# Kernel tuning notes

Hardware: AMD Instinct MI355X
Metric: run time of the kernel (lower is better)

The kernel has to match this reference:

```python
import jax, jax.numpy as jnp
import numpy as np

N_NODES = 70000
N_EDGES = 2_000_000
IN_CH, FEAT_CH, OUT_CH = 1044, 128, 3


def _gcn_norm(src_sl, dst_sl, n_nodes, dtype):
    # PyG gcn_norm with add_self_loops=True, edge_weight=1:
    # deg over target nodes, norm = deg^-1/2[src] * deg^-1/2[dst]
    deg = jax.ops.segment_sum(jnp.ones(src_sl.shape[0], dtype=dtype), dst_sl,
                              num_segments=n_nodes)
    dinv = jnp.where(deg > 0, jax.lax.rsqrt(deg), jnp.zeros((), dtype))
    return dinv[src_sl] * dinv[dst_sl]


def _gcn_layer(x, src_sl, dst_sl, norm, W, b, n_nodes):
    h = x @ W                                  # [N, out] linear transform first
    msg = h[src_sl] * norm[:, None]            # gather + scale
    out = jax.ops.segment_sum(msg, dst_sl, num_segments=n_nodes)  # scatter-add
    return out + b


def setup_inputs() -> dict:
    key = jax.random.key(0)
    ks = jax.random.split(key, 6)
    features = jax.random.normal(ks[0], (N_NODES, IN_CH), dtype=jnp.float32)
    edges = jax.random.randint(ks[1], (2, N_EDGES), 0, N_NODES, dtype=jnp.int64)
    edges2 = jax.random.randint(ks[2], (2, N_EDGES), 0, N_NODES, dtype=jnp.int64)
    edge_features = jax.random.normal(ks[3], (N_EDGES,), dtype=jnp.float32)
    W1 = jax.random.normal(ks[4], (IN_CH, FEAT_CH), dtype=jnp.float32) * (1.0 / np.sqrt(IN_CH))
    b1 = jnp.zeros((FEAT_CH,), dtype=jnp.float32)
    W2 = jax.random.normal(ks[5], (FEAT_CH, OUT_CH), dtype=jnp.float32) * (1.0 / np.sqrt(FEAT_CH))
    b2 = jnp.zeros((OUT_CH,), dtype=jnp.float32)
    return {"features": features, "edges": edges, "edges2": edges2,
            "edge_features": edge_features, "W1": W1, "b1": b1, "W2": W2, "b2": b2}


def reference(features, edges, edges2, edge_features, W1, b1, W2, b2):
    # edge_features is discarded by the module (set to None); edges2 unused.
    n = features.shape[0]
    loop = jnp.arange(n, dtype=edges.dtype)
    src_sl = jnp.concatenate([edges[0], loop])  # self-loops appended
    dst_sl = jnp.concatenate([edges[1], loop])
    norm = _gcn_norm(src_sl, dst_sl, n, features.dtype)
    x = _gcn_layer(features, src_sl, dst_sl, norm, W1, b1, n)
    x = jax.nn.relu(x)
    # dropout is identity in eval mode (deterministic reference)
    return _gcn_layer(x, src_sl, dst_sl, norm, W2, b2, n)
```

## Files before the change

### kernel.cpp

```cpp
#include <hip/hip_runtime.h>
#include <hip/hip_bf16.h>

#define K_IN   1044
#define N_FEAT 128
#define KPAD2  1088
#define NST2   17
#define BM     96

#define NB     512
#define BWMAX  256
#define EPB    8192

typedef __attribute__((ext_vector_type(8))) short short8;
typedef __attribute__((ext_vector_type(4))) float f32x4;

__device__ __forceinline__ ushort f2bf(float f) {
  unsigned x = __float_as_uint(f);
  x += 0x7fffu + ((x >> 16) & 1u);
  return (ushort)(x >> 16);
}
__device__ __forceinline__ uint pkbf(float lo, float hi) {
  __hip_bfloat162 h = __float22bfloat162_rn(make_float2(lo, hi));
  return *reinterpret_cast<uint*>(&h);
}
__device__ __forceinline__ float bflo(uint v) { return __uint_as_float(v << 16); }
__device__ __forceinline__ float bfhi(uint v) { return __uint_as_float(v & 0xFFFF0000u); }

__device__ __forceinline__ uint divbw(uint d, uint M32) { return __umulhi(d, M32); }

__device__ __forceinline__ void gld16(const void* g, void* l) {
  __builtin_amdgcn_global_load_lds(
      (const __attribute__((address_space(1))) unsigned int*)g,
      (__attribute__((address_space(3))) unsigned int*)l, 16, 0, 0);
}


__global__ __launch_bounds__(256) void convw1_hist_kernel(const float* __restrict__ W1,
                                                          ushort* __restrict__ W1T,
                                                          const int* __restrict__ dst,
                                                          int* __restrict__ pbc,
                                                          int E, int bw, uint M32,
                                                          int convBlocks, int eblocks) {
  if ((int)blockIdx.x < convBlocks) {
    int idx = blockIdx.x * 256 + threadIdx.x;
    if (idx >= N_FEAT * KPAD2) return;
    int col = idx / KPAD2, k = idx - col * KPAD2;
    int kk = k & ~63;
    int jp = (k >> 3) & 7;
    int e  = k & 7;
    int jl = jp ^ (col & 7);
    int ksrc = kk + 8 * jl + e;
    W1T[idx] = (ksrc < K_IN) ? f2bf(W1[(size_t)ksrc * N_FEAT + col]) : (ushort)0;
  } else {
    __shared__ int h[NB];
    const int t = threadIdx.x;
    const int blk = blockIdx.x - convBlocks;
    for (int i = t; i < NB; i += 256) h[i] = 0;
    __syncthreads();
    const int e0 = blk * EPB;
    const int e1 = min(e0 + EPB, E);
    for (int e = e0 + t; e < e1; e += 256) atomicAdd(&h[divbw((uint)dst[e], M32)], 1);
    __syncthreads();
    for (int i = t; i < NB; i += 256) pbc[i * eblocks + blk] = h[i];
  }
}

__global__ __launch_bounds__(256) void csr_scan_bucket_kernel(int* __restrict__ pbc,
                                                              int* __restrict__ bt,
                                                              int eblocks) {
  __shared__ int sc[256];
  const int b = blockIdx.x;
  const int t = threadIdx.x;
  int v = (t < eblocks) ? pbc[(size_t)b * eblocks + t] : 0;
  sc[t] = v;
  __syncthreads();
  for (int off = 1; off < 256; off <<= 1) {
    int x = (t >= off) ? sc[t - off] : 0;
    __syncthreads();
    sc[t] += x;
    __syncthreads();
  }
  if (t < eblocks) pbc[(size_t)b * eblocks + t] = sc[t] - v;
  if (t == 255) bt[b] = sc[255];
}

__global__ __launch_bounds__(256) void csr_stage_kernel(const int* __restrict__ src,
                                                        const int* __restrict__ dst,
                                                        const int* __restrict__ pbc,
                                                        const int* __restrict__ bt,
                                                        uint* __restrict__ staging, int E, int bw,
                                                        uint M32, int eblocks) {
  __shared__ int sc[256];
  __shared__ int cur[NB];
  const int t = threadIdx.x;
  const int blk = blockIdx.x;
  int v0 = bt[2 * t], v1 = bt[2 * t + 1];
  int s = v0 + v1;
  sc[t] = s;
  __syncthreads();
  for (int off = 1; off < 256; off <<= 1) {
    int x = (t >= off) ? sc[t - off] : 0;
    __syncthreads();
    sc[t] += x;
    __syncthreads();
  }
  int excl = sc[t] - s;
  cur[2 * t]     = excl      + pbc[(size_t)(2 * t) * eblocks + blk];
  cur[2 * t + 1] = excl + v0 + pbc[(size_t)(2 * t + 1) * eblocks + blk];
  __syncthreads();
  const int e0 = blk * EPB;
  const int e1 = min(e0 + EPB, E);
  for (int e = e0 + t; e < e1; e += 256) {
    int d = dst[e];
    int b = (int)divbw((uint)d, M32);
    int p = atomicAdd(&cur[b], 1);
    staging[p] = ((uint)src[e] << 8) | (uint)(d - b * bw);
  }
}

__global__ __launch_bounds__(256) void csr_final_kernel(const uint* __restrict__ staging,
                                                        const int* __restrict__ bt,
                                                        int* __restrict__ row_ptr,
                                                        int* __restrict__ sorted_src,
                                                        float* __restrict__ dinv,
                                                        int N, int bw, int E) {
  __shared__ int hist[BWMAX];
  __shared__ int sc[256];
  __shared__ int bb[NB];
  const int b = blockIdx.x;
  const int t = threadIdx.x;
  if (b == 0 && t == 0) row_ptr[N] = E;

  {
    int v0 = bt[2 * t], v1 = bt[2 * t + 1];
    int s = v0 + v1;
    sc[t] = s;
    __syncthreads();
    for (int off = 1; off < 256; off <<= 1) {
      int x = (t >= off) ? sc[t - off] : 0;
      __syncthreads();
      sc[t] += x;
      __syncthreads();
    }
    int excl = sc[t] - s;
    bb[2 * t]     = excl;
    bb[2 * t + 1] = excl + v0;
    __syncthreads();
  }

  const int node0 = b * bw;
  const int nn = min(bw, N - node0);
  if (nn <= 0) return;
  const int base = bb[b];
  const int cnt  = bt[b];

  for (int i = t; i < BWMAX; i += 256) hist[i] = 0;
  __syncthreads();
  for (int i = t; i < cnt; i += 256)
    atomicAdd(&hist[staging[base + i] & 255u], 1);
  __syncthreads();
  int v = (t < nn) ? hist[t] : 0;
  if (t < nn) dinv[node0 + t] = rsqrtf((float)(v + 1));
  sc[t] = v;
  __syncthreads();
  for (int off = 1; off < 256; off <<= 1) {
    int x = (t >= off) ? sc[t - off] : 0;
    __syncthreads();
    sc[t] += x;
    __syncthreads();
  }
  int excl = sc[t] - v;
  if (t < nn) row_ptr[node0 + t] = base + excl;
  if (t < nn) hist[t] = excl;
  __syncthreads();
  for (int i = t; i < cnt; i += 256) {
    uint p = staging[base + i];
    int c = atomicAdd(&hist[p & 255u], 1);
    sorted_src[base + c] = (int)(p >> 8);
  }
}


__global__ __launch_bounds__(256) void gemm1_mfma_kernel(const float* __restrict__ X,
                                                         const ushort* __restrict__ W1T,
                                                         const float* __restrict__ dinv,
                                                         ushort* __restrict__ G1, int M) {
  __shared__ float  Af[2][BM * 64];
  __shared__ ushort Bsb[2][128 * 64];

  const int t = threadIdx.x;
  const int row0 = blockIdx.x * BM;
  const int w = t >> 6, l = t & 63;
  const int w24 = w * 24, w32 = w * 32;
  const int Mm1 = M - 1;

  const int wm = w >> 1, wn = w & 1;
  const int lr = l & 15, g = l >> 4;

  f32x4 acc[3][4] = {};

  auto stage = [&](int s, int buf) {
    const int kk = s * 64;
    #pragma unroll
    for (int i = 0; i < 6; i++) {
      int r  = w24 + 4 * i + (l >> 4);
      int jl = (l & 15) ^ (r & 15);
      int grow = min(row0 + r, Mm1);
      int gk   = min(kk + 4 * jl, K_IN - 4);
      gld16(X + (size_t)grow * K_IN + gk, (void*)&Af[buf][(w24 + 4 * i) * 64]);
    }
    #pragma unroll
    for (int i = 0; i < 4; i++) {
      int c = w32 + 8 * i + (l >> 3);
      gld16(W1T + (size_t)c * KPAD2 + kk + 8 * (l & 7),
            (void*)&Bsb[buf][(w32 + 8 * i) * 64]);
    }
  };

  stage(0, 0);
  __syncthreads();

  int cur = 0;
  #pragma unroll 1
  for (int s = 0; s < NST2; s++) {
    if (s + 1 < NST2) stage(s + 1, cur ^ 1);

    #pragma unroll
    for (int ss = 0; ss < 2; ss++) {
      short8 af[3], bfr[4];
      #pragma unroll
      for (int m = 0; m < 3; m++) {
        const int row = wm * 48 + m * 16 + lr;
        const float* rp = &Af[cur][row * 64];
        const int c0 = (ss * 8 + 2 * g)     ^ (row & 15);
        const int c1 = (ss * 8 + 2 * g + 1) ^ (row & 15);
        float4 a0 = *(const float4*)&rp[c0 * 4];
        float4 a1 = *(const float4*)&rp[c1 * 4];
        uint4 uu = make_uint4(pkbf(a0.x, a0.y), pkbf(a0.z, a0.w),
                              pkbf(a1.x, a1.y), pkbf(a1.z, a1.w));
        af[m] = *(short8*)&uu;
      }
      #pragma unroll
      for (int n = 0; n < 4; n++) {
        const int col = wn * 64 + n * 16 + lr;
        const int cB = (ss * 4 + g) ^ (col & 7);
        bfr[n] = *(const short8*)&Bsb[cur][col * 64 + cB * 8];
      }
      #pragma unroll
      for (int m = 0; m < 3; m++)
        #pragma unroll
        for (int n = 0; n < 4; n++)
          acc[m][n] = __builtin_amdgcn_mfma_f32_16x16x32_bf16(af[m], bfr[n], acc[m][n], 0, 0, 0);
    }

    __syncthreads();
    cur ^= 1;
  }

  const int rbase = row0 + wm * 48 + g * 4;
  const int cbase = wn * 64 + lr;
  #pragma unroll
  for (int m = 0; m < 3; m++) {
    #pragma unroll
    for (int r = 0; r < 4; r++) {
      int row = rbase + m * 16 + r;
      if (row < M) {
        float dv = dinv[row];
        #pragma unroll
        for (int n = 0; n < 4; n++)
          G1[(size_t)row * N_FEAT + cbase + n * 16] = f2bf(dv * acc[m][n][r]);
      }
    }
  }
}


__global__ __launch_bounds__(256) void agg1mm_kernel(const ushort* __restrict__ G1,
                                                     const int* __restrict__ row_ptr,
                                                     const int* __restrict__ sorted_src,
                                                     const float* __restrict__ dinv,
                                                     const float* __restrict__ b1,
                                                     const float* __restrict__ W2,
                                                     float* __restrict__ G2, int N) {
  const int w = (blockIdx.x * blockDim.x + threadIdx.x) >> 6;
  const int lane = threadIdx.x & 63;
  if (w >= N) return;
  const int beg = row_ptr[w], end = row_ptr[w + 1];
  const uint* g1u = (const uint*)G1;
  const int co = lane;

  uint vs = g1u[((size_t)w << 6) + co];
  float a0 = bflo(vs), a1 = bfhi(vs);

  int e = beg;
  for (; e + 16 <= end; e += 16) {
    int s[16];
    #pragma unroll
    for (int i = 0; i < 16; i++) s[i] = sorted_src[e + i];
    uint v[16];
    #pragma unroll
    for (int i = 0; i < 16; i++) v[i] = g1u[((size_t)s[i] << 6) + co];
    #pragma unroll
    for (int i = 0; i < 16; i++) { a0 += bflo(v[i]); a1 += bfhi(v[i]); }
  }
  for (; e + 4 <= end; e += 4) {
    int s[4];
    #pragma unroll
    for (int i = 0; i < 4; i++) s[i] = sorted_src[e + i];
    uint v[4];
    #pragma unroll
    for (int i = 0; i < 4; i++) v[i] = g1u[((size_t)s[i] << 6) + co];
    #pragma unroll
    for (int i = 0; i < 4; i++) { a0 += bflo(v[i]); a1 += bfhi(v[i]); }
  }
  for (; e < end; e++) {
    uint v = g1u[((size_t)sorted_src[e] << 6) + co];
    a0 += bflo(v); a1 += bfhi(v);
  }

  const float di = dinv[w];
  float r0 = fmaxf(fmaf(di, a0, b1[2 * co + 0]), 0.f);
  float r1 = fmaxf(fmaf(di, a1, b1[2 * co + 1]), 0.f);

  const float* wrow = W2 + 6 * co;
  float s0 = r0 * wrow[0] + r1 * wrow[3];
  float s1 = r0 * wrow[1] + r1 * wrow[4];
  float s2 = r0 * wrow[2] + r1 * wrow[5];
  #pragma unroll
  for (int off = 32; off > 0; off >>= 1) {
    s0 += __shfl_down(s0, off);
    s1 += __shfl_down(s1, off);
    s2 += __shfl_down(s2, off);
  }
  if (lane == 0) {
    *(float4*)&G2[(size_t)w * 4] = make_float4(di * s0, di * s1, di * s2, 0.f);
  }
}


__global__ __launch_bounds__(256) void agg2_kernel(const float* __restrict__ G2,
                                                   const int* __restrict__ row_ptr,
                                                   const int* __restrict__ sorted_src,
                                                   const float* __restrict__ dinv,
                                                   const float* __restrict__ b2,
                                                   float* __restrict__ out, int N) {
  int t = blockIdx.x * blockDim.x + threadIdx.x;
  int node = t >> 4, lane = t & 15;
  if (node >= N) return;
  int beg = row_ptr[node], end = row_ptr[node + 1];
  float a0 = 0.f, a1 = 0.f, a2 = 0.f;
  for (int e = beg + lane; e < end; e += 16) {
    float4 v = *(const float4*)&G2[(size_t)sorted_src[e] * 4];
    a0 += v.x; a1 += v.y; a2 += v.z;
  }
  #pragma unroll
  for (int off = 8; off > 0; off >>= 1) {
    a0 += __shfl_down(a0, off, 16);
    a1 += __shfl_down(a1, off, 16);
    a2 += __shfl_down(a2, off, 16);
  }
  if (lane == 0) {
    float di = dinv[node];
    float4 self = *(const float4*)&G2[(size_t)node * 4];
    out[node * 3 + 0] = di * (a0 + self.x) + b2[0];
    out[node * 3 + 1] = di * (a1 + self.y) + b2[1];
    out[node * 3 + 2] = di * (a2 + self.z) + b2[2];
  }
}


extern "C" void kernel_launch(void* const* d_in, const int* in_sizes, int n_in,
                              void* d_out, int out_size, void* d_ws, size_t ws_size,
                              hipStream_t stream) {
  const float* features = (const float*)d_in[0];
  const int*   edges    = (const int*)d_in[1];
  const float* W1 = (const float*)d_in[4];
  const float* b1 = (const float*)d_in[5];
  const float* W2 = (const float*)d_in[6];
  const float* b2 = (const float*)d_in[7];
  float* out = (float*)d_out;

  const int N = in_sizes[0] / K_IN;
  const int E = in_sizes[1] / 2;
  const int* src = edges;
  const int* dst = edges + E;
  const int bw = (N + NB - 1) / NB;
  const uint M32 = (uint)((0x100000000ULL + (unsigned long long)bw - 1) / (unsigned long long)bw);

  char* ws = (char*)d_ws;
  size_t off = 0;
  auto alloc = [&](size_t bytes) {
    void* p = ws + off;
    off += (bytes + 255) & ~(size_t)255;
    return p;
  };
  const int eblocks = (E + EPB - 1) / EPB;

  int*    pbc           = (int*)   alloc((size_t)NB * eblocks * sizeof(int));
  int*    bt            = (int*)   alloc((size_t)NB * sizeof(int));
  int*    row_ptr       = (int*)   alloc((size_t)(N + 1) * sizeof(int));
  float*  dinv          = (float*) alloc((size_t)N * sizeof(float));
  uint*   staging       = (uint*)  alloc((size_t)E * sizeof(uint));
  int*    sorted_src    = (int*)   alloc((size_t)E * sizeof(int));
  ushort* G1            = (ushort*)alloc((size_t)N * N_FEAT * sizeof(ushort));
  float*  G2            = (float*) alloc((size_t)N * 4 * sizeof(float));
  ushort* W1T           = (ushort*)alloc((size_t)N_FEAT * KPAD2 * sizeof(ushort));
  (void)ws_size;

  const int convBlocks = (N_FEAT * KPAD2 + 255) / 256;

  convw1_hist_kernel<<<convBlocks + eblocks, 256, 0, stream>>>(W1, W1T, dst, pbc, E, bw, M32, convBlocks, eblocks);
  csr_scan_bucket_kernel<<<NB, 256, 0, stream>>>(pbc, bt, eblocks);
  csr_stage_kernel<<<eblocks, 256, 0, stream>>>(src, dst, pbc, bt, staging, E, bw, M32, eblocks);
  csr_final_kernel<<<NB, 256, 0, stream>>>(staging, bt, row_ptr, sorted_src, dinv, N, bw, E);
  gemm1_mfma_kernel<<<(N + BM - 1) / BM, 256, 0, stream>>>(features, W1T, dinv, G1, N);
  agg1mm_kernel<<<((size_t)N * 64 + 255) / 256, 256, 0, stream>>>(G1, row_ptr, sorted_src, dinv, b1, W2, G2, N);
  agg2_kernel<<<((size_t)N * 16 + 255) / 256, 256, 0, stream>>>(G2, row_ptr, sorted_src, dinv, b2, out, N);
}
```

Measured before the change: 234.0 us.

## Fuse four CSR-build kernels into one persistent kernel with grid barriers

Merges the W1 conversion/histogram, bucket scan, staging scatter and final per-bucket sort kernels into a single 512-block persistent kernel that separates phases with a software grid barrier built on global atomics. The aim is to remove three kernel launch gaps and their tail effects between small CSR phases. It adds a memset for the barrier counter, relies on all 512 blocks being co-resident to avoid deadlock, and adds barrier spin and fence costs.

```diff
diff --git a/kernel.cpp b/kernel.cpp
--- a/kernel.cpp
+++ b/kernel.cpp
@@ -7,9 +7,10 @@
 #define NST2   17
 #define BM     96
 
-#define NB     512
-#define BWMAX  256
-#define EPB    8192
+#define NB      512
+#define BWMAX   256
+#define EPB     8192
+#define CSRGRID 512
 
 typedef __attribute__((ext_vector_type(8))) short short8;
 typedef __attribute__((ext_vector_type(4))) float f32x4;
@@ -34,102 +35,110 @@
       (__attribute__((address_space(3))) unsigned int*)l, 16, 0, 0);
 }
 
-
-__global__ __launch_bounds__(256) void convw1_hist_kernel(const float* __restrict__ W1,
-                                                          ushort* __restrict__ W1T,
-                                                          const int* __restrict__ dst,
-                                                          int* __restrict__ pbc,
-                                                          int E, int bw, uint M32,
-                                                          int convBlocks, int eblocks) {
-  if ((int)blockIdx.x < convBlocks) {
-    int idx = blockIdx.x * 256 + threadIdx.x;
-    if (idx >= N_FEAT * KPAD2) return;
-    int col = idx / KPAD2, k = idx - col * KPAD2;
-    int kk = k & ~63;
-    int jp = (k >> 3) & 7;
-    int e  = k & 7;
-    int jl = jp ^ (col & 7);
-    int ksrc = kk + 8 * jl + e;
-    W1T[idx] = (ksrc < K_IN) ? f2bf(W1[(size_t)ksrc * N_FEAT + col]) : (ushort)0;
-  } else {
-    __shared__ int h[NB];
-    const int t = threadIdx.x;
-    const int blk = blockIdx.x - convBlocks;
-    for (int i = t; i < NB; i += 256) h[i] = 0;
+__device__ __forceinline__ void gridbar(int* __restrict__ bar) {
+  __syncthreads();
+  if (threadIdx.x == 0) {
+    __threadfence();
+    int g = __hip_atomic_load(&bar[1], __ATOMIC_RELAXED, __HIP_MEMORY_SCOPE_AGENT);
+    int a = __hip_atomic_fetch_add(&bar[0], 1, __ATOMIC_ACQ_REL, __HIP_MEMORY_SCOPE_AGENT);
+    if (a == CSRGRID - 1) {
+      __hip_atomic_store(&bar[0], 0, __ATOMIC_RELAXED, __HIP_MEMORY_SCOPE_AGENT);
+      __hip_atomic_fetch_add(&bar[1], 1, __ATOMIC_ACQ_REL, __HIP_MEMORY_SCOPE_AGENT);
+    } else {
+      while (__hip_atomic_load(&bar[1], __ATOMIC_ACQUIRE, __HIP_MEMORY_SCOPE_AGENT) == g)
+        __builtin_amdgcn_s_sleep(8);
+    }
+    __threadfence();
+  }
+  __syncthreads();
+}
+
+
+__global__ __launch_bounds__(256) void csr_mega_kernel(const float* __restrict__ W1,
+                                                       ushort* __restrict__ W1T,
+                                                       const int* __restrict__ src,
+                                                       const int* __restrict__ dst,
+                                                       int* __restrict__ pbc,
+                                                       int* __restrict__ bt,
+                                                       uint* __restrict__ staging,
+                                                       int* __restrict__ row_ptr,
+                                                       int* __restrict__ sorted_src,
+                                                       float* __restrict__ dinv,
+                                                       int N, int E, int bw, uint M32,
+                                                       int convBlocks, int eblocks,
+                                                       int* __restrict__ bar) {
+  __shared__ int h[NB];
+  __shared__ int sc[256];
+  __shared__ int hist2[BWMAX];
+  const int t = threadIdx.x;
+  const int blk = blockIdx.x;
+
+  for (int vb = blk; vb < convBlocks + eblocks; vb += CSRGRID) {
+    if (vb < convBlocks) {
+      int idx = vb * 256 + t;
+      if (idx < N_FEAT * KPAD2) {
+        int col = idx / KPAD2, k = idx - col * KPAD2;
+        int kk = k & ~63;
+        int jp = (k >> 3) & 7;
+        int e  = k & 7;
+        int jl = jp ^ (col & 7);
+        int ksrc = kk + 8 * jl + e;
+        W1T[idx] = (ksrc < K_IN) ? f2bf(W1[(size_t)ksrc * N_FEAT + col]) : (ushort)0;
+      }
+    } else {
+      const int c = vb - convBlocks;
+      for (int i = t; i < NB; i += 256) h[i] = 0;
+      __syncthreads();
+      const int e0 = c * EPB;
+      const int e1 = min(e0 + EPB, E);
+      for (int e = e0 + t; e < e1; e += 256) atomicAdd(&h[divbw((uint)dst[e], M32)], 1);
+      __syncthreads();
+      for (int i = t; i < NB; i += 256) pbc[(size_t)i * eblocks + c] = h[i];
+      __syncthreads();
+    }
+  }
+  gridbar(bar);
+
+  {
+    int v = (t < eblocks) ? pbc[(size_t)blk * eblocks + t] : 0;
+    sc[t] = v;
+    __syncthreads();
+    for (int off = 1; off < 256; off <<= 1) {
+      int x = (t >= off) ? sc[t - off] : 0;
+      __syncthreads();
+      sc[t] += x;
+      __syncthreads();
+    }
+    if (t < eblocks) pbc[(size_t)blk * eblocks + t] = sc[t] - v;
+    if (t == 255) bt[blk] = sc[255];
+  }
+  gridbar(bar);
+
+  if (blk < eblocks) {
+    int v0 = bt[2 * t], v1 = bt[2 * t + 1];
+    int s = v0 + v1;
+    sc[t] = s;
+    __syncthreads();
+    for (int off = 1; off < 256; off <<= 1) {
+      int x = (t >= off) ? sc[t - off] : 0;
+      __syncthreads();
+      sc[t] += x;
+      __syncthreads();
+    }
+    int excl = sc[t] - s;
+    h[2 * t]     = excl      + pbc[(size_t)(2 * t) * eblocks + blk];
+    h[2 * t + 1] = excl + v0 + pbc[(size_t)(2 * t + 1) * eblocks + blk];
     __syncthreads();
     const int e0 = blk * EPB;
     const int e1 = min(e0 + EPB, E);
-    for (int e = e0 + t; e < e1; e += 256) atomicAdd(&h[divbw((uint)dst[e], M32)], 1);
-    __syncthreads();
-    for (int i = t; i < NB; i += 256) pbc[i * eblocks + blk] = h[i];
-  }
-}
-
-__global__ __launch_bounds__(256) void csr_scan_bucket_kernel(int* __restrict__ pbc,
-                                                              int* __restrict__ bt,
-                                                              int eblocks) {
-  __shared__ int sc[256];
-  const int b = blockIdx.x;
-  const int t = threadIdx.x;
-  int v = (t < eblocks) ? pbc[(size_t)b * eblocks + t] : 0;
-  sc[t] = v;
-  __syncthreads();
-  for (int off = 1; off < 256; off <<= 1) {
-    int x = (t >= off) ? sc[t - off] : 0;
-    __syncthreads();
-    sc[t] += x;
-    __syncthreads();
-  }
-  if (t < eblocks) pbc[(size_t)b * eblocks + t] = sc[t] - v;
-  if (t == 255) bt[b] = sc[255];
-}
-
-__global__ __launch_bounds__(256) void csr_stage_kernel(const int* __restrict__ src,
-                                                        const int* __restrict__ dst,
-                                                        const int* __restrict__ pbc,
-                                                        const int* __restrict__ bt,
-                                                        uint* __restrict__ staging, int E, int bw,
-                                                        uint M32, int eblocks) {
-  __shared__ int sc[256];
-  __shared__ int cur[NB];
-  const int t = threadIdx.x;
-  const int blk = blockIdx.x;
-  int v0 = bt[2 * t], v1 = bt[2 * t + 1];
-  int s = v0 + v1;
-  sc[t] = s;
-  __syncthreads();
-  for (int off = 1; off < 256; off <<= 1) {
-    int x = (t >= off) ? sc[t - off] : 0;
-    __syncthreads();
-    sc[t] += x;
-    __syncthreads();
-  }
-  int excl = sc[t] - s;
-  cur[2 * t]     = excl      + pbc[(size_t)(2 * t) * eblocks + blk];
-  cur[2 * t + 1] = excl + v0 + pbc[(size_t)(2 * t + 1) * eblocks + blk];
-  __syncthreads();
-  const int e0 = blk * EPB;
-  const int e1 = min(e0 + EPB, E);
-  for (int e = e0 + t; e < e1; e += 256) {
-    int d = dst[e];
-    int b = (int)divbw((uint)d, M32);
-    int p = atomicAdd(&cur[b], 1);
-    staging[p] = ((uint)src[e] << 8) | (uint)(d - b * bw);
-  }
-}
-
-__global__ __launch_bounds__(256) void csr_final_kernel(const uint* __restrict__ staging,
-                                                        const int* __restrict__ bt,
-                                                        int* __restrict__ row_ptr,
-                                                        int* __restrict__ sorted_src,
-                                                        float* __restrict__ dinv,
-                                                        int N, int bw, int E) {
-  __shared__ int hist[BWMAX];
-  __shared__ int sc[256];
-  __shared__ int bb[NB];
-  const int b = blockIdx.x;
-  const int t = threadIdx.x;
-  if (b == 0 && t == 0) row_ptr[N] = E;
+    for (int e = e0 + t; e < e1; e += 256) {
+      int d = dst[e];
+      int b = (int)divbw((uint)d, M32);
+      int p = atomicAdd(&h[b], 1);
+      staging[p] = ((uint)src[e] << 8) | (uint)(d - b * bw);
+    }
+  }
+  gridbar(bar);
 
   {
     int v0 = bt[2 * t], v1 = bt[2 * t + 1];
@@ -143,23 +152,23 @@
       __syncthreads();
     }
     int excl = sc[t] - s;
-    bb[2 * t]     = excl;
-    bb[2 * t + 1] = excl + v0;
-    __syncthreads();
-  }
-
-  const int node0 = b * bw;
+    h[2 * t]     = excl;
+    h[2 * t + 1] = excl + v0;
+    __syncthreads();
+  }
+  if (blk == 0 && t == 0) row_ptr[N] = E;
+  const int node0 = blk * bw;
   const int nn = min(bw, N - node0);
   if (nn <= 0) return;
-  const int base = bb[b];
-  const int cnt  = bt[b];
-
-  for (int i = t; i < BWMAX; i += 256) hist[i] = 0;
+  const int base = h[blk];
+  const int cnt  = bt[blk];
+
+  for (int i = t; i < BWMAX; i += 256) hist2[i] = 0;
   __syncthreads();
   for (int i = t; i < cnt; i += 256)
-    atomicAdd(&hist[staging[base + i] & 255u], 1);
-  __syncthreads();
-  int v = (t < nn) ? hist[t] : 0;
+    atomicAdd(&hist2[staging[base + i] & 255u], 1);
+  __syncthreads();
+  int v = (t < nn) ? hist2[t] : 0;
   if (t < nn) dinv[node0 + t] = rsqrtf((float)(v + 1));
   sc[t] = v;
   __syncthreads();
@@ -171,11 +180,11 @@
   }
   int excl = sc[t] - v;
   if (t < nn) row_ptr[node0 + t] = base + excl;
-  if (t < nn) hist[t] = excl;
+  if (t < nn) hist2[t] = excl;
   __syncthreads();
   for (int i = t; i < cnt; i += 256) {
     uint p = staging[base + i];
-    int c = atomicAdd(&hist[p & 255u], 1);
+    int c = atomicAdd(&hist2[p & 255u], 1);
     sorted_src[base + c] = (int)(p >> 8);
   }
 }
@@ -396,6 +405,7 @@
   };
   const int eblocks = (E + EPB - 1) / EPB;
 
+  int*    bar           = (int*)   alloc(64);
   int*    pbc           = (int*)   alloc((size_t)NB * eblocks * sizeof(int));
   int*    bt            = (int*)   alloc((size_t)NB * sizeof(int));
   int*    row_ptr       = (int*)   alloc((size_t)(N + 1) * sizeof(int));
@@ -409,10 +419,10 @@
 
   const int convBlocks = (N_FEAT * KPAD2 + 255) / 256;
 
-  convw1_hist_kernel<<<convBlocks + eblocks, 256, 0, stream>>>(W1, W1T, dst, pbc, E, bw, M32, convBlocks, eblocks);
-  csr_scan_bucket_kernel<<<NB, 256, 0, stream>>>(pbc, bt, eblocks);
-  csr_stage_kernel<<<eblocks, 256, 0, stream>>>(src, dst, pbc, bt, staging, E, bw, M32, eblocks);
-  csr_final_kernel<<<NB, 256, 0, stream>>>(staging, bt, row_ptr, sorted_src, dinv, N, bw, E);
+  hipMemsetAsync(bar, 0, 64, stream);
+  csr_mega_kernel<<<CSRGRID, 256, 0, stream>>>(W1, W1T, src, dst, pbc, bt, staging,
+                                               row_ptr, sorted_src, dinv,
+                                               N, E, bw, M32, convBlocks, eblocks, bar);
   gemm1_mfma_kernel<<<(N + BM - 1) / BM, 256, 0, stream>>>(features, W1T, dinv, G1, N);
   agg1mm_kernel<<<((size_t)N * 64 + 255) / 256, 256, 0, stream>>>(G1, row_ptr, sorted_src, dinv, b1, W2, G2, N);
   agg2_kernel<<<((size_t)N * 16 + 255) / 256, 256, 0, stream>>>(G2, row_ptr, sorted_src, dinv, b2, out, N);
```

Measured after the change: 626.9 us. 2.68x slower.

## Merge CSR staging with GEMM1 launch and move source-degree scaling into aggregation

Applied to the files above, without the earlier changes.

The CSR staging pass and the first GEMM now run in one launch, with block ID ranges selecting the role, so the bandwidth-bound GEMM can overlap the atomic-heavy edge bucketing. To drop GEMM1's dependency on dinv, the per-source dinv scaling moves out of the GEMM epilogue into agg1mm, which now gathers dinv[src] per edge and uses FMA. This removes one launch and the serialization between CSR build and GEMM, but adds 2M extra scattered dinv loads in aggregation and a bf16 rounding change, since G1 is stored unscaled.

```diff
diff --git a/kernel.cpp b/kernel.cpp
--- a/kernel.cpp
+++ b/kernel.cpp
@@ -84,54 +84,26 @@
   if (t == 255) bt[b] = sc[255];
 }
 
-__global__ __launch_bounds__(256) void csr_stage_kernel(const int* __restrict__ src,
-                                                        const int* __restrict__ dst,
-                                                        const int* __restrict__ pbc,
-                                                        const int* __restrict__ bt,
-                                                        uint* __restrict__ staging, int E, int bw,
-                                                        uint M32, int eblocks) {
-  __shared__ int sc[256];
-  __shared__ int cur[NB];
+
+__global__ __launch_bounds__(256) void stage_gemm1_kernel(const int* __restrict__ src,
+                                                          const int* __restrict__ dst,
+                                                          const int* __restrict__ pbc,
+                                                          const int* __restrict__ bt,
+                                                          uint* __restrict__ staging,
+                                                          const float* __restrict__ X,
+                                                          const ushort* __restrict__ W1T,
+                                                          ushort* __restrict__ G1,
+                                                          int M, int E, int bw, uint M32,
+                                                          int eblocks) {
+  __shared__ float  Af[2][BM * 64];
+  __shared__ ushort Bsb[2][128 * 64];
+
   const int t = threadIdx.x;
-  const int blk = blockIdx.x;
-  int v0 = bt[2 * t], v1 = bt[2 * t + 1];
-  int s = v0 + v1;
-  sc[t] = s;
-  __syncthreads();
-  for (int off = 1; off < 256; off <<= 1) {
-    int x = (t >= off) ? sc[t - off] : 0;
-    __syncthreads();
-    sc[t] += x;
-    __syncthreads();
-  }
-  int excl = sc[t] - s;
-  cur[2 * t]     = excl      + pbc[(size_t)(2 * t) * eblocks + blk];
-  cur[2 * t + 1] = excl + v0 + pbc[(size_t)(2 * t + 1) * eblocks + blk];
-  __syncthreads();
-  const int e0 = blk * EPB;
-  const int e1 = min(e0 + EPB, E);
-  for (int e = e0 + t; e < e1; e += 256) {
-    int d = dst[e];
-    int b = (int)divbw((uint)d, M32);
-    int p = atomicAdd(&cur[b], 1);
-    staging[p] = ((uint)src[e] << 8) | (uint)(d - b * bw);
-  }
-}
-
-__global__ __launch_bounds__(256) void csr_final_kernel(const uint* __restrict__ staging,
-                                                        const int* __restrict__ bt,
-                                                        int* __restrict__ row_ptr,
-                                                        int* __restrict__ sorted_src,
-                                                        float* __restrict__ dinv,
-                                                        int N, int bw, int E) {
-  __shared__ int hist[BWMAX];
-  __shared__ int sc[256];
-  __shared__ int bb[NB];
-  const int b = blockIdx.x;
-  const int t = threadIdx.x;
-  if (b == 0 && t == 0) row_ptr[N] = E;
-
-  {
+
+  if ((int)blockIdx.x < eblocks) {
+    int* sc  = (int*)&Bsb[0][0];
+    int* cur = (int*)&Af[0][0];
+    const int blk = blockIdx.x;
     int v0 = bt[2 * t], v1 = bt[2 * t + 1];
     int s = v0 + v1;
     sc[t] = s;
@@ -143,53 +115,21 @@
       __syncthreads();
     }
     int excl = sc[t] - s;
-    bb[2 * t]     = excl;
-    bb[2 * t + 1] = excl + v0;
-    __syncthreads();
-  }
-
-  const int node0 = b * bw;
-  const int nn = min(bw, N - node0);
-  if (nn <= 0) return;
-  const int base = bb[b];
-  const int cnt  = bt[b];
-
-  for (int i = t; i < BWMAX; i += 256) hist[i] = 0;
-  __syncthreads();
-  for (int i = t; i < cnt; i += 256)
-    atomicAdd(&hist[staging[base + i] & 255u], 1);
-  __syncthreads();
-  int v = (t < nn) ? hist[t] : 0;
-  if (t < nn) dinv[node0 + t] = rsqrtf((float)(v + 1));
-  sc[t] = v;
-  __syncthreads();
-  for (int off = 1; off < 256; off <<= 1) {
-    int x = (t >= off) ? sc[t - off] : 0;
-    __syncthreads();
-    sc[t] += x;
-    __syncthreads();
-  }
-  int excl = sc[t] - v;
-  if (t < nn) row_ptr[node0 + t] = base + excl;
-  if (t < nn) hist[t] = excl;
-  __syncthreads();
-  for (int i = t; i < cnt; i += 256) {
-    uint p = staging[base + i];
-    int c = atomicAdd(&hist[p & 255u], 1);
-    sorted_src[base + c] = (int)(p >> 8);
-  }
-}
-
-
-__global__ __launch_bounds__(256) void gemm1_mfma_kernel(const float* __restrict__ X,
-                                                         const ushort* __restrict__ W1T,
-                                                         const float* __restrict__ dinv,
-                                                         ushort* __restrict__ G1, int M) {
-  __shared__ float  Af[2][BM * 64];
-  __shared__ ushort Bsb[2][128 * 64];
-
-  const int t = threadIdx.x;
-  const int row0 = blockIdx.x * BM;
+    cur[2 * t]     = excl      + pbc[(size_t)(2 * t) * eblocks + blk];
+    cur[2 * t + 1] = excl + v0 + pbc[(size_t)(2 * t + 1) * eblocks + blk];
+    __syncthreads();
+    const int e0 = blk * EPB;
+    const int e1 = min(e0 + EPB, E);
+    for (int e = e0 + t; e < e1; e += 256) {
+      int d = dst[e];
+      int b = (int)divbw((uint)d, M32);
+      int p = atomicAdd(&cur[b], 1);
+      staging[p] = ((uint)src[e] << 8) | (uint)(d - b * bw);
+    }
+    return;
+  }
+
+  const int row0 = ((int)blockIdx.x - eblocks) * BM;
   const int w = t >> 6, l = t & 63;
   const int w24 = w * 24, w32 = w * 32;
   const int Mm1 = M - 1;
@@ -265,12 +205,73 @@
     for (int r = 0; r < 4; r++) {
       int row = rbase + m * 16 + r;
       if (row < M) {
-        float dv = dinv[row];
         #pragma unroll
         for (int n = 0; n < 4; n++)
-          G1[(size_t)row * N_FEAT + cbase + n * 16] = f2bf(dv * acc[m][n][r]);
+          G1[(size_t)row * N_FEAT + cbase + n * 16] = f2bf(acc[m][n][r]);
       }
     }
+  }
+}
+
+__global__ __launch_bounds__(256) void csr_final_kernel(const uint* __restrict__ staging,
+                                                        const int* __restrict__ bt,
+                                                        int* __restrict__ row_ptr,
+                                                        int* __restrict__ sorted_src,
+                                                        float* __restrict__ dinv,
+                                                        int N, int bw, int E) {
+  __shared__ int hist[BWMAX];
+  __shared__ int sc[256];
+  __shared__ int bb[NB];
+  const int b = blockIdx.x;
+  const int t = threadIdx.x;
+  if (b == 0 && t == 0) row_ptr[N] = E;
+
+  {
+    int v0 = bt[2 * t], v1 = bt[2 * t + 1];
+    int s = v0 + v1;
+    sc[t] = s;
+    __syncthreads();
+    for (int off = 1; off < 256; off <<= 1) {
+      int x = (t >= off) ? sc[t - off] : 0;
+      __syncthreads();
+      sc[t] += x;
+      __syncthreads();
+    }
+    int excl = sc[t] - s;
+    bb[2 * t]     = excl;
+    bb[2 * t + 1] = excl + v0;
+    __syncthreads();
+  }
+
+  const int node0 = b * bw;
+  const int nn = min(bw, N - node0);
+  if (nn <= 0) return;
+  const int base = bb[b];
+  const int cnt  = bt[b];
+
+  for (int i = t; i < BWMAX; i += 256) hist[i] = 0;
+  __syncthreads();
+  for (int i = t; i < cnt; i += 256)
+    atomicAdd(&hist[staging[base + i] & 255u], 1);
+  __syncthreads();
+  int v = (t < nn) ? hist[t] : 0;
+  if (t < nn) dinv[node0 + t] = rsqrtf((float)(v + 1));
+  sc[t] = v;
+  __syncthreads();
+  for (int off = 1; off < 256; off <<= 1) {
+    int x = (t >= off) ? sc[t - off] : 0;
+    __syncthreads();
+    sc[t] += x;
+    __syncthreads();
+  }
+  int excl = sc[t] - v;
+  if (t < nn) row_ptr[node0 + t] = base + excl;
+  if (t < nn) hist[t] = excl;
+  __syncthreads();
+  for (int i = t; i < cnt; i += 256) {
+    uint p = staging[base + i];
+    int c = atomicAdd(&hist[p & 255u], 1);
+    sorted_src[base + c] = (int)(p >> 8);
   }
 }
 
@@ -288,37 +289,42 @@
   const int beg = row_ptr[w], end = row_ptr[w + 1];
   const uint* g1u = (const uint*)G1;
   const int co = lane;
+  const float di = dinv[w];
 
   uint vs = g1u[((size_t)w << 6) + co];
-  float a0 = bflo(vs), a1 = bfhi(vs);
+  float a0 = di * bflo(vs), a1 = di * bfhi(vs);
 
   int e = beg;
   for (; e + 16 <= end; e += 16) {
     int s[16];
     #pragma unroll
     for (int i = 0; i < 16; i++) s[i] = sorted_src[e + i];
+    float dv[16];
     uint v[16];
     #pragma unroll
-    for (int i = 0; i < 16; i++) v[i] = g1u[((size_t)s[i] << 6) + co];
-    #pragma unroll
-    for (int i = 0; i < 16; i++) { a0 += bflo(v[i]); a1 += bfhi(v[i]); }
+    for (int i = 0; i < 16; i++) { v[i] = g1u[((size_t)s[i] << 6) + co]; dv[i] = dinv[s[i]]; }
+    #pragma unroll
+    for (int i = 0; i < 16; i++) { a0 = fmaf(dv[i], bflo(v[i]), a0); a1 = fmaf(dv[i], bfhi(v[i]), a1); }
   }
   for (; e + 4 <= end; e += 4) {
     int s[4];
     #pragma unroll
     for (int i = 0; i < 4; i++) s[i] = sorted_src[e + i];
+    float dv[4];
     uint v[4];
     #pragma unroll
-    for (int i = 0; i < 4; i++) v[i] = g1u[((size_t)s[i] << 6) + co];
-    #pragma unroll
-    for (int i = 0; i < 4; i++) { a0 += bflo(v[i]); a1 += bfhi(v[i]); }
+    for (int i = 0; i < 4; i++) { v[i] = g1u[((size_t)s[i] << 6) + co]; dv[i] = dinv[s[i]]; }
+    #pragma unroll
+    for (int i = 0; i < 4; i++) { a0 = fmaf(dv[i], bflo(v[i]), a0); a1 = fmaf(dv[i], bfhi(v[i]), a1); }
   }
   for (; e < end; e++) {
-    uint v = g1u[((size_t)sorted_src[e] << 6) + co];
-    a0 += bflo(v); a1 += bfhi(v);
-  }
-
-  const float di = dinv[w];
+    int s = sorted_src[e];
+    uint v = g1u[((size_t)s << 6) + co];
+    float dv = dinv[s];
+    a0 = fmaf(dv, bflo(v), a0);
+    a1 = fmaf(dv, bfhi(v), a1);
+  }
+
   float r0 = fmaxf(fmaf(di, a0, b1[2 * co + 0]), 0.f);
   float r1 = fmaxf(fmaf(di, a1, b1[2 * co + 1]), 0.f);
 
@@ -408,12 +414,14 @@
   (void)ws_size;
 
   const int convBlocks = (N_FEAT * KPAD2 + 255) / 256;
+  const int gemmBlocks = (N + BM - 1) / BM;
 
   convw1_hist_kernel<<<convBlocks + eblocks, 256, 0, stream>>>(W1, W1T, dst, pbc, E, bw, M32, convBlocks, eblocks);
   csr_scan_bucket_kernel<<<NB, 256, 0, stream>>>(pbc, bt, eblocks);
-  csr_stage_kernel<<<eblocks, 256, 0, stream>>>(src, dst, pbc, bt, staging, E, bw, M32, eblocks);
+  stage_gemm1_kernel<<<eblocks + gemmBlocks, 256, 0, stream>>>(src, dst, pbc, bt, staging,
+                                                               features, W1T, G1,
+                                                               N, E, bw, M32, eblocks);
   csr_final_kernel<<<NB, 256, 0, stream>>>(staging, bt, row_ptr, sorted_src, dinv, N, bw, E);
-  gemm1_mfma_kernel<<<(N + BM - 1) / BM, 256, 0, stream>>>(features, W1T, dinv, G1, N);
   agg1mm_kernel<<<((size_t)N * 64 + 255) / 256, 256, 0, stream>>>(G1, row_ptr, sorted_src, dinv, b1, W2, G2, N);
   agg2_kernel<<<((size_t)N * 16 + 255) / 256, 256, 0, stream>>>(G2, row_ptr, sorted_src, dinv, b2, out, N);
 }
```

Measured after the change: 244.3 us. 1.04x slower.
